# Kernel tuning notes

Hardware: AMD Instinct MI355X
Metric: run time of the kernel (lower is better)

The kernel has to match this reference:

```python
import jax, jax.numpy as jnp
import numpy as np

S, N, D = 65536, 8192, 128  # images, texts, embed dim


def setup_inputs() -> dict:
    key = jax.random.key(0)
    k1, k2, k3 = jax.random.split(key, 3)
    return {
        "image_features": jax.random.normal(k1, (S, D), dtype=jnp.float32),
        "text_features": jax.random.normal(k2, (N, D), dtype=jnp.float32),
        "key": jax.random.randint(k3, (S,), 0, N),
        "logit_scale": jnp.asarray(10.0, dtype=jnp.float32),  # already exponentiated temperature
        "logit_bias": jnp.asarray(-10.0, dtype=jnp.float32),
    }


def _l2norm(x):
    return x / (jnp.linalg.norm(x, ord=2, axis=-1, keepdims=True) + 1e-12)


def reference(image_features, text_features, key, logit_scale, logit_bias):
    s = image_features.shape[0]
    n = text_features.shape[0]
    zimg = _l2norm(image_features)           # (s, d)
    ztxt = _l2norm(text_features)            # (n, d)

    # True-positive logits: only the diagonal gather of the full (s, n) matmul is used,
    # so compute it directly as a row-wise dot product.
    tp_logits = jnp.einsum("sd,sd->s", zimg, ztxt[key]) * logit_scale + logit_bias
    pot_losses = jax.nn.softplus(-tp_logits)  # (s,)

    # Segmented argmin over images grouped by their text key (pick_best_candidate=True).
    seg_min = jax.ops.segment_min(pot_losses, key, num_segments=n)        # (n,)
    counts = jax.ops.segment_sum(jnp.ones((s,), jnp.int32), key, num_segments=n)
    valid = counts > 0                                                    # (n,)
    is_min = pot_losses == seg_min[key]
    cand_idx = jnp.where(is_min, jnp.arange(s), s)                        # first-occurrence tie-break
    best = jax.ops.segment_min(cand_idx, key, num_segments=n)             # (n,)
    best = jnp.where(valid, best, 0)

    zimg_sel = jnp.where(valid[:, None], zimg[best], 0.0)                 # (n, d)

    logits = zimg_sel @ ztxt.T * logit_scale + logit_bias                 # (n, n)
    diag = jnp.eye(n, dtype=bool)
    # labels*logits == logits on diagonal, -logits off-diagonal; softplus(-labels*logits):
    terms = jax.nn.softplus(jnp.where(diag, -logits, logits))
    mask = valid[:, None] & valid[None, :]
    num_valid = jnp.sum(valid)
    loss = jnp.sum(jnp.where(mask, terms, 0.0)) / jnp.maximum(num_valid, 1).astype(terms.dtype)
    return loss
```

## Files before the change

kernel.cpp:

```cpp
#include <hip/hip_runtime.h>
#include <stdint.h>

#define D 128

typedef __attribute__((ext_vector_type(4))) float float4v;
typedef long long frag8;

__device__ __forceinline__ float hw_exp2(float x) { return __builtin_amdgcn_exp2f(x); }
__device__ __forceinline__ float hw_log2(float x) { return __builtin_amdgcn_logf(x); }

__device__ __forceinline__ float softplus_fast(float x) {
    float e = hw_exp2(x * 1.44269504f);
    return 0.69314718f * hw_log2(1.0f + e);
}

__device__ __forceinline__ unsigned short f2fp8x2(float x, float y) {
    int p = __builtin_amdgcn_cvt_pk_fp8_f32(x, y, 0, false);
    return (unsigned short)(p & 0xFFFF);
}

__device__ __forceinline__ float dot4(float4 a, float4 b) {
    return a.x * b.x + a.y * b.y + a.z * b.z + a.w * b.w;
}

__device__ __forceinline__ void gload_lds16(const uint8_t* g, uint8_t* l) {
    __builtin_amdgcn_global_load_lds(
        (const __attribute__((address_space(1))) void*)g,
        (__attribute__((address_space(3))) void*)l, 16, 0, 0);
}

__device__ __forceinline__ int swz_col(int c, int row) {
    return c ^ ((row & 15) << 3);
}

__global__ __launch_bounds__(256) void k_prep(const float* __restrict__ img,
                                              const float* __restrict__ txt,
                                              const int* __restrict__ key,
                                              const float* __restrict__ sc,
                                              const float* __restrict__ bi,
                                              uint8_t* __restrict__ ztxt_f8,
                                              unsigned long long* __restrict__ packed,
                                              int nPack, int S) {
    const int t = threadIdx.x;
    if ((int)blockIdx.x < nPack) {
        int wave = t >> 6, lane = t & 63;
        int n = blockIdx.x * 4 + wave;
        const float2 v = *(const float2*)(txt + (size_t)n * D + lane * 2);
        float ss = v.x * v.x + v.y * v.y;
        #pragma unroll
        for (int off = 32; off; off >>= 1) ss += __shfl_xor(ss, off);
        float inv = 1.0f / (sqrtf(ss) + 1e-12f);
        *(unsigned short*)(ztxt_f8 + (size_t)n * D + swz_col(lane * 2, n)) =
            f2fp8x2(v.x * inv, v.y * inv);
    } else {
        int grp = t >> 4, gl = t & 15;
        int s = ((int)blockIdx.x - nPack) * 16 + grp;
        if (s < S) {
            int k = key[s];
            const float4* ia = (const float4*)(img + (size_t)s * D);
            const float4* tb = (const float4*)(txt + (size_t)k * D);
            float4 a0 = ia[gl], a1 = ia[16 + gl];
            float4 b0 = tb[gl], b1 = tb[16 + gl];
            float ss = dot4(a0, a0) + dot4(a1, a1);
            float dt = dot4(a0, b0) + dot4(a1, b1);
            float tt = dot4(b0, b0) + dot4(b1, b1);
            #pragma unroll
            for (int off = 8; off; off >>= 1) {
                ss += __shfl_xor(ss, off);
                dt += __shfl_xor(dt, off);
                tt += __shfl_xor(tt, off);
            }
            if (gl == 0) {
                float inv_i = 1.0f / (sqrtf(ss) + 1e-12f);
                float inv_t = 1.0f / (sqrtf(tt) + 1e-12f);
                float tp = dt * inv_i * inv_t * (*sc) + (*bi);
                float pot = softplus_fast(-tp);
                unsigned long long p =
                    ((unsigned long long)__float_as_uint(pot) << 32) | (unsigned int)s;
                atomicMin(&packed[k], p);
            }
        }
    }
}

__global__ __launch_bounds__(256) void k_select(const float* __restrict__ img,
                                               const unsigned long long* __restrict__ packed,
                                               uint8_t* __restrict__ zsel_f8,
                                               float* __restrict__ validF,
                                               double* __restrict__ partial) {
    int t = threadIdx.x;
    if (blockIdx.x == 0) partial[t] = 0.0;
    int wave = t >> 6;
    int lane = t & 63;
    int n = blockIdx.x * 4 + wave;
    unsigned long long p = packed[n];
    bool valid = (p != ~0ull);
    if (!valid) {
        if (lane == 0) validF[n] = 0.0f;
        *(unsigned short*)(zsel_f8 + (size_t)n * D + swz_col(lane * 2, n)) = 0;
        return;
    }
    int s = (int)(unsigned int)(p & 0xFFFFFFFFull);
    const float2 a = *(const float2*)(img + (size_t)s * D + lane * 2);
    float ss = a.x * a.x + a.y * a.y;
    #pragma unroll
    for (int off = 32; off; off >>= 1) ss += __shfl_xor(ss, off);
    float inv = 1.0f / (sqrtf(ss) + 1e-12f);
    *(unsigned short*)(zsel_f8 + (size_t)n * D + swz_col(lane * 2, n)) =
        f2fp8x2(a.x * inv, a.y * inv);
    if (lane == 0) validF[n] = 1.0f;
}

__global__ __launch_bounds__(256, 3) void k_gemm(const uint8_t* __restrict__ A,
                                                 const uint8_t* __restrict__ B,
                                                 const float* __restrict__ validF,
                                                 const float* __restrict__ sc,
                                                 const float* __restrict__ bi,
                                                 double* __restrict__ partial) {
    __shared__ __align__(16) uint8_t As[128 * 128];
    __shared__ __align__(16) uint8_t Bs[2][128 * 128];
    __shared__ float vI[128];
    __shared__ float vJ[512];
    __shared__ float wsum[4];

    const int t = threadIdx.x;
    const int i0 = blockIdx.y * 128;
    const int j0 = blockIdx.x * 512;

    vJ[t] = validF[j0 + t];
    vJ[t + 256] = validF[j0 + t + 256];
    if (t < 128) vI[t] = validF[i0 + t];

    const int wave = t >> 6, lane = t & 63;
    const int wm = (wave >> 1) * 64;
    const int wn = (wave & 1) * 64;
    const int lr = lane & 15;
    const int kq = (lane >> 4) * 8;
    const int swz = lr << 3;

    const uint8_t* gA = A + (size_t)i0 * D;
    const uint8_t* gB = B + (size_t)j0 * D;

    {
        #pragma unroll
        for (int j = 0; j < 4; ++j) {
            int L = wave * 4096 + j * 1024;
            gload_lds16(gA + L + lane * 16, As + L);
            gload_lds16(gB + L + lane * 16, Bs[0] + L);
        }
    }
    __syncthreads();

    const float scale = *sc, bias = *bi;
    const float sl = scale * 1.44269504f, bl = bias * 1.44269504f;
    const int rb = (lane >> 4) * 4;
    float viv[4][4];
    #pragma unroll
    for (int mi = 0; mi < 4; ++mi)
        #pragma unroll
        for (int r = 0; r < 4; ++r) viv[mi][r] = vI[wm + mi * 16 + rb + r];

    float sum = 0.0f;

    #pragma unroll
    for (int ji = 0; ji < 4; ++ji) {
        if (ji < 3) {
            const uint8_t* gS = gB + (ji + 1) * (128 * 128);
            #pragma unroll
            for (int j = 0; j < 4; ++j) {
                int L = wave * 4096 + j * 1024;
                gload_lds16(gS + L + lane * 16, Bs[(ji + 1) & 1] + L);
            }
        }
        const uint8_t* Bc = Bs[ji & 1];

        float4v acc[4][4];
        #pragma unroll
        for (int mi = 0; mi < 4; ++mi)
            #pragma unroll
            for (int ni = 0; ni < 4; ++ni)
                acc[mi][ni] = (float4v){0.f, 0.f, 0.f, 0.f};

        #pragma unroll
        for (int k0 = 0; k0 < 128; k0 += 32) {
            const int col = (k0 + kq) ^ swz;
            frag8 bf[4];
            #pragma unroll
            for (int ni = 0; ni < 4; ++ni)
                bf[ni] = *(const frag8*)(Bc + (wn + ni * 16 + lr) * 128 + col);
            #pragma unroll
            for (int mi = 0; mi < 4; ++mi) {
                frag8 af = *(const frag8*)(As + (wm + mi * 16 + lr) * 128 + col);
                #pragma unroll
                for (int ni = 0; ni < 4; ++ni)
                    acc[mi][ni] = __builtin_amdgcn_mfma_f32_16x16x32_fp8_fp8(
                        af, bf[ni], acc[mi][ni], 0, 0, 0);
            }
        }

        float vjv[4];
        #pragma unroll
        for (int ni = 0; ni < 4; ++ni) vjv[ni] = vJ[ji * 128 + wn + ni * 16 + lr];

        const int jt = blockIdx.x * 4 + ji;
        if (jt != (int)blockIdx.y) {
            #pragma unroll
            for (int ni = 0; ni < 4; ++ni) {
                float s = 0.0f;
                #pragma unroll
                for (int mi = 0; mi < 4; ++mi)
                    #pragma unroll
                    for (int r = 0; r < 4; ++r) {
                        float u = hw_exp2(fmaf(acc[mi][ni][r], sl, bl));
                        s = fmaf(u, viv[mi][r], s);
                    }
                sum = fmaf(s, vjv[ni], sum);
            }
        } else {
            #pragma unroll
            for (int ni = 0; ni < 4; ++ni) {
                float s = 0.0f;
                const int lj = wn + ni * 16 + lr;
                #pragma unroll
                for (int mi = 0; mi < 4; ++mi)
                    #pragma unroll
                    for (int r = 0; r < 4; ++r) {
                        const int li = wm + mi * 16 + rb + r;
                        float l = fmaf(acc[mi][ni][r], scale, bias);
                        float u = hw_exp2(-fabsf(l) * 1.44269504f);
                        float g = fmaxf(l, 0.0f) + fmaf(-0.5f * u, u, u);
                        if (li == lj) g -= l;
                        s = fmaf(g, viv[mi][r], s);
                    }
                sum = fmaf(s, vjv[ni], sum);
            }
        }
        if (ji < 3) __syncthreads();
    }

    #pragma unroll
    for (int off = 32; off; off >>= 1) sum += __shfl_xor(sum, off);
    if (lane == 0) wsum[wave] = sum;
    __syncthreads();
    if (t == 0) {
        float bs = wsum[0] + wsum[1] + wsum[2] + wsum[3];
        atomicAdd(&partial[(blockIdx.y * gridDim.x + blockIdx.x) & 255], (double)bs);
    }
}

__global__ __launch_bounds__(256) void k_final(const double* __restrict__ partial,
                                               const float* __restrict__ validF,
                                               float* __restrict__ out, int N) {
    __shared__ float wsum[4];
    __shared__ double dsum[4];
    int wave = threadIdx.x >> 6, lane = threadIdx.x & 63;
    float s = 0.0f;
    for (int i = threadIdx.x; i < N; i += 256) s += validF[i];
    double d = partial[threadIdx.x];
    #pragma unroll
    for (int off = 32; off; off >>= 1) {
        s += __shfl_xor(s, off);
        d += __shfl_xor(d, off);
    }
    if (lane == 0) { wsum[wave] = s; dsum[wave] = d; }
    __syncthreads();
    if (threadIdx.x == 0) {
        float nv = wsum[0] + wsum[1] + wsum[2] + wsum[3];
        if (nv < 1.0f) nv = 1.0f;
        double tot = dsum[0] + dsum[1] + dsum[2] + dsum[3];
        out[0] = (float)(tot / (double)nv);
    }
}

extern "C" void kernel_launch(void* const* d_in, const int* in_sizes, int n_in,
                              void* d_out, int out_size, void* d_ws, size_t ws_size,
                              hipStream_t stream) {
    const float* img = (const float*)d_in[0];
    const float* txt = (const float*)d_in[1];
    const int*   key = (const int*)d_in[2];
    const float* sc  = (const float*)d_in[3];
    const float* bi  = (const float*)d_in[4];
    float* out = (float*)d_out;

    const int S = in_sizes[2];
    const int N = in_sizes[1] / D;

    char* ws = (char*)d_ws;
    size_t off = 0;
    auto carve = [&](size_t bytes) {
        void* p = ws + off;
        off = (off + bytes + 255) & ~(size_t)255;
        return p;
    };
    uint8_t*            ztxt_f8 = (uint8_t*)carve((size_t)N * D);
    uint8_t*            zsel_f8 = (uint8_t*)carve((size_t)N * D);
    unsigned long long* packed  = (unsigned long long*)carve((size_t)N * sizeof(unsigned long long));
    float*              validF  = (float*)carve((size_t)N * sizeof(float));
    double*             partial = (double*)carve(256 * sizeof(double));

    hipMemsetAsync(packed, 0xFF, (size_t)N * sizeof(unsigned long long), stream);

    const int nPack = N / 4;
    k_prep<<<nPack + (S + 15) / 16, 256, 0, stream>>>(img, txt, key, sc, bi,
                                                      ztxt_f8, packed, nPack, S);
    k_select<<<N / 4, 256, 0, stream>>>(img, packed, zsel_f8, validF, partial);
    dim3 g(N / 512, N / 128);
    k_gemm<<<g, 256, 0, stream>>>(zsel_f8, ztxt_f8, validF, sc, bi, partial);
    k_final<<<1, 256, 0, stream>>>(partial, validF, out, N);
}
```

Measured before the change: 114.6 us.

## Fuse row selection into GEMM prologue and final reduction into last block

Removes the k_select and k_final kernels. Each GEMM block now gathers its 128 selected image rows, normalizes them and converts them to swizzled FP8 directly into LDS, and reads validity from the packed argmin array. The last GEMM block, found with an atomic counter, performs the final reduction. This saves two launches and the round trip of zsel/validF through global memory. In exchange, every column-block redundantly recomputes the same A rows (16x duplication), and the gather adds latency before the first MMA.

New measurement: 132.2 us. 15.4% more time.

```diff
diff --git a/kernel.cpp b/kernel.cpp
--- a/kernel.cpp
+++ b/kernel.cpp
@@ -40,9 +40,15 @@
                                               const float* __restrict__ bi,
                                               uint8_t* __restrict__ ztxt_f8,
                                               unsigned long long* __restrict__ packed,
+                                              double* __restrict__ partial,
+                                              unsigned int* __restrict__ counter,
                                               int nPack, int S) {
     const int t = threadIdx.x;
     if ((int)blockIdx.x < nPack) {
+        if (blockIdx.x == 0) {
+            partial[t] = 0.0;
+            if (t == 0) { partial[256] = 0.0; *counter = 0u; }
+        }
         int wave = t >> 6, lane = t & 63;
         int n = blockIdx.x * 4 + wave;
         const float2 v = *(const float2*)(txt + (size_t)n * D + lane * 2);
@@ -83,73 +89,80 @@
     }
 }
 
-__global__ __launch_bounds__(256) void k_select(const float* __restrict__ img,
-                                               const unsigned long long* __restrict__ packed,
-                                               uint8_t* __restrict__ zsel_f8,
-                                               float* __restrict__ validF,
-                                               double* __restrict__ partial) {
-    int t = threadIdx.x;
-    if (blockIdx.x == 0) partial[t] = 0.0;
-    int wave = t >> 6;
-    int lane = t & 63;
-    int n = blockIdx.x * 4 + wave;
-    unsigned long long p = packed[n];
-    bool valid = (p != ~0ull);
-    if (!valid) {
-        if (lane == 0) validF[n] = 0.0f;
-        *(unsigned short*)(zsel_f8 + (size_t)n * D + swz_col(lane * 2, n)) = 0;
-        return;
-    }
-    int s = (int)(unsigned int)(p & 0xFFFFFFFFull);
-    const float2 a = *(const float2*)(img + (size_t)s * D + lane * 2);
-    float ss = a.x * a.x + a.y * a.y;
-    #pragma unroll
-    for (int off = 32; off; off >>= 1) ss += __shfl_xor(ss, off);
-    float inv = 1.0f / (sqrtf(ss) + 1e-12f);
-    *(unsigned short*)(zsel_f8 + (size_t)n * D + swz_col(lane * 2, n)) =
-        f2fp8x2(a.x * inv, a.y * inv);
-    if (lane == 0) validF[n] = 1.0f;
-}
-
-__global__ __launch_bounds__(256, 3) void k_gemm(const uint8_t* __restrict__ A,
+__global__ __launch_bounds__(256, 3) void k_gemm(const float* __restrict__ img,
                                                  const uint8_t* __restrict__ B,
-                                                 const float* __restrict__ validF,
+                                                 const unsigned long long* __restrict__ packed,
                                                  const float* __restrict__ sc,
                                                  const float* __restrict__ bi,
-                                                 double* __restrict__ partial) {
+                                                 double* __restrict__ partial,
+                                                 unsigned int* __restrict__ counter,
+                                                 float* __restrict__ out, int N) {
     __shared__ __align__(16) uint8_t As[128 * 128];
     __shared__ __align__(16) uint8_t Bs[2][128 * 128];
     __shared__ float vI[128];
     __shared__ float vJ[512];
     __shared__ float wsum[4];
+    __shared__ float wcnt[4];
+    __shared__ double dred[4];
+    __shared__ int lastB;
 
     const int t = threadIdx.x;
     const int i0 = blockIdx.y * 128;
     const int j0 = blockIdx.x * 512;
 
-    vJ[t] = validF[j0 + t];
-    vJ[t + 256] = validF[j0 + t + 256];
-    if (t < 128) vI[t] = validF[i0 + t];
-
     const int wave = t >> 6, lane = t & 63;
+    const uint8_t* gB = B + (size_t)j0 * D;
+
+    {
+        #pragma unroll
+        for (int j = 0; j < 4; ++j) {
+            int L = wave * 4096 + j * 1024;
+            gload_lds16(gB + L + lane * 16, Bs[0] + L);
+        }
+    }
+
+    vJ[t]       = (packed[j0 + t] != ~0ull) ? 1.0f : 0.0f;
+    vJ[t + 256] = (packed[j0 + 256 + t] != ~0ull) ? 1.0f : 0.0f;
+
+    {
+        const int grp = t >> 4, gl = t & 15;
+        unsigned long long pk[8];
+        #pragma unroll
+        for (int it = 0; it < 8; ++it) pk[it] = packed[i0 + it * 16 + grp];
+        #pragma unroll
+        for (int it = 0; it < 8; ++it) {
+            const int row = it * 16 + grp;
+            const unsigned long long p = pk[it];
+            const bool valid = (p != ~0ull);
+            uint32_t o0 = 0, o1 = 0;
+            if (valid) {
+                int s = (int)(unsigned int)(p & 0xFFFFFFFFull);
+                const float4* ia = (const float4*)(img + (size_t)s * D);
+                float4 a0 = ia[gl], a1 = ia[16 + gl];
+                float ss = dot4(a0, a0) + dot4(a1, a1);
+                #pragma unroll
+                for (int off = 8; off; off >>= 1) ss += __shfl_xor(ss, off);
+                float inv = 1.0f / (sqrtf(ss) + 1e-12f);
+                unsigned short p01 = f2fp8x2(a0.x * inv, a0.y * inv);
+                unsigned short p23 = f2fp8x2(a0.z * inv, a0.w * inv);
+                unsigned short p45 = f2fp8x2(a1.x * inv, a1.y * inv);
+                unsigned short p67 = f2fp8x2(a1.z * inv, a1.w * inv);
+                o0 = (uint32_t)p01 | ((uint32_t)p23 << 16);
+                o1 = (uint32_t)p45 | ((uint32_t)p67 << 16);
+            }
+            if (gl == 0) vI[row] = valid ? 1.0f : 0.0f;
+            const int sw = (row & 15) << 3;
+            *(uint32_t*)(As + row * 128 + ((4 * gl) ^ sw)) = o0;
+            *(uint32_t*)(As + row * 128 + ((64 + 4 * gl) ^ sw)) = o1;
+        }
+    }
+    __syncthreads();
+
     const int wm = (wave >> 1) * 64;
     const int wn = (wave & 1) * 64;
     const int lr = lane & 15;
     const int kq = (lane >> 4) * 8;
     const int swz = lr << 3;
-
-    const uint8_t* gA = A + (size_t)i0 * D;
-    const uint8_t* gB = B + (size_t)j0 * D;
-
-    {
-        #pragma unroll
-        for (int j = 0; j < 4; ++j) {
-            int L = wave * 4096 + j * 1024;
-            gload_lds16(gA + L + lane * 16, As + L);
-            gload_lds16(gB + L + lane * 16, Bs[0] + L);
-        }
-    }
-    __syncthreads();
 
     const float scale = *sc, bias = *bi;
     const float sl = scale * 1.44269504f, bl = bias * 1.44269504f;
@@ -238,37 +251,38 @@
         if (ji < 3) __syncthreads();
     }
 
+    float vc = (blockIdx.x == 0 && t < 128) ? vI[t] : 0.0f;
     #pragma unroll
-    for (int off = 32; off; off >>= 1) sum += __shfl_xor(sum, off);
-    if (lane == 0) wsum[wave] = sum;
+    for (int off = 32; off; off >>= 1) {
+        sum += __shfl_xor(sum, off);
+        vc  += __shfl_xor(vc, off);
+    }
+    if (lane == 0) { wsum[wave] = sum; wcnt[wave] = vc; }
     __syncthreads();
     if (t == 0) {
         float bs = wsum[0] + wsum[1] + wsum[2] + wsum[3];
         atomicAdd(&partial[(blockIdx.y * gridDim.x + blockIdx.x) & 255], (double)bs);
-    }
-}
-
-__global__ __launch_bounds__(256) void k_final(const double* __restrict__ partial,
-                                               const float* __restrict__ validF,
-                                               float* __restrict__ out, int N) {
-    __shared__ float wsum[4];
-    __shared__ double dsum[4];
-    int wave = threadIdx.x >> 6, lane = threadIdx.x & 63;
-    float s = 0.0f;
-    for (int i = threadIdx.x; i < N; i += 256) s += validF[i];
-    double d = partial[threadIdx.x];
-    #pragma unroll
-    for (int off = 32; off; off >>= 1) {
-        s += __shfl_xor(s, off);
-        d += __shfl_xor(d, off);
-    }
-    if (lane == 0) { wsum[wave] = s; dsum[wave] = d; }
+        if (blockIdx.x == 0) {
+            float bc = wcnt[0] + wcnt[1] + wcnt[2] + wcnt[3];
+            atomicAdd(&partial[256], (double)bc);
+        }
+        __threadfence();
+        unsigned int v = atomicAdd(counter, 1u);
+        lastB = (v == gridDim.x * gridDim.y - 1u);
+    }
     __syncthreads();
-    if (threadIdx.x == 0) {
-        float nv = wsum[0] + wsum[1] + wsum[2] + wsum[3];
-        if (nv < 1.0f) nv = 1.0f;
-        double tot = dsum[0] + dsum[1] + dsum[2] + dsum[3];
-        out[0] = (float)(tot / (double)nv);
+    if (lastB) {
+        double ds = atomicAdd(&partial[t], 0.0);
+        #pragma unroll
+        for (int off = 32; off; off >>= 1) ds += __shfl_xor(ds, off);
+        if (lane == 0) dred[wave] = ds;
+        __syncthreads();
+        if (t == 0) {
+            double tot = dred[0] + dred[1] + dred[2] + dred[3];
+            float nv = (float)atomicAdd(&partial[256], 0.0);
+            if (nv < 1.0f) nv = 1.0f;
+            out[0] = (float)(tot / (double)nv);
+        }
     }
 }
 
@@ -293,18 +307,17 @@
         return p;
     };
     uint8_t*            ztxt_f8 = (uint8_t*)carve((size_t)N * D);
-    uint8_t*            zsel_f8 = (uint8_t*)carve((size_t)N * D);
     unsigned long long* packed  = (unsigned long long*)carve((size_t)N * sizeof(unsigned long long));
-    float*              validF  = (float*)carve((size_t)N * sizeof(float));
-    double*             partial = (double*)carve(256 * sizeof(double));
+    double*             partial = (double*)carve(257 * sizeof(double));
+    unsigned int*       counter = (unsigned int*)carve(sizeof(unsigned int));
 
     hipMemsetAsync(packed, 0xFF, (size_t)N * sizeof(unsigned long long), stream);
 
     const int nPack = N / 4;
     k_prep<<<nPack + (S + 15) / 16, 256, 0, stream>>>(img, txt, key, sc, bi,
-                                                      ztxt_f8, packed, nPack, S);
-    k_select<<<N / 4, 256, 0, stream>>>(img, packed, zsel_f8, validF, partial);
+                                                      ztxt_f8, packed, partial,
+                                                      counter, nPack, S);
     dim3 g(N / 512, N / 128);
-    k_gemm<<<g, 256, 0, stream>>>(zsel_f8, ztxt_f8, validF, sc, bi, partial);
-    k_final<<<1, 256, 0, stream>>>(partial, validF, out, N);
-}
+    k_gemm<<<g, 256, 0, stream>>>(img, ztxt_f8, packed, sc, bi,
+                                  partial, counter, out, N);
+}
```

## Make GEMM kernel persistent with atomic work queue over tiles

Applied to the files above, without the earlier changes.

Replaces the 2D grid of 1024 GEMM tiles with a persistent grid of 768 blocks that pull tile indices from a global atomic counter, which k_select resets. The tile order is column-major (by varies fastest) so consecutive blocks share the same B strip. The aim is to cut block launch overhead and tail imbalance, and to improve L2 reuse of B. In exchange it adds an atomic and a barrier per tile, and it loses the overlap of the next tile's initial loads with the previous tile's epilogue.

After: 124.5 us. +8.7%, slower.

```diff
diff --git a/kernel.cpp b/kernel.cpp
--- a/kernel.cpp
+++ b/kernel.cpp
@@ -87,9 +87,13 @@
                                                const unsigned long long* __restrict__ packed,
                                                uint8_t* __restrict__ zsel_f8,
                                                float* __restrict__ validF,
-                                               double* __restrict__ partial) {
+                                               double* __restrict__ partial,
+                                               unsigned int* __restrict__ queue) {
     int t = threadIdx.x;
-    if (blockIdx.x == 0) partial[t] = 0.0;
+    if (blockIdx.x == 0) {
+        partial[t] = 0.0;
+        if (t == 0) *queue = 0u;
+    }
     int wave = t >> 6;
     int lane = t & 63;
     int n = blockIdx.x * 4 + wave;
@@ -116,126 +120,141 @@
                                                  const float* __restrict__ validF,
                                                  const float* __restrict__ sc,
                                                  const float* __restrict__ bi,
-                                                 double* __restrict__ partial) {
+                                                 double* __restrict__ partial,
+                                                 unsigned int* __restrict__ queue,
+                                                 int N) {
     __shared__ __align__(16) uint8_t As[128 * 128];
     __shared__ __align__(16) uint8_t Bs[2][128 * 128];
     __shared__ float vI[128];
     __shared__ float vJ[512];
     __shared__ float wsum[4];
+    __shared__ int wsh;
 
     const int t = threadIdx.x;
-    const int i0 = blockIdx.y * 128;
-    const int j0 = blockIdx.x * 512;
-
-    vJ[t] = validF[j0 + t];
-    vJ[t + 256] = validF[j0 + t + 256];
-    if (t < 128) vI[t] = validF[i0 + t];
-
     const int wave = t >> 6, lane = t & 63;
     const int wm = (wave >> 1) * 64;
     const int wn = (wave & 1) * 64;
     const int lr = lane & 15;
     const int kq = (lane >> 4) * 8;
     const int swz = lr << 3;
-
-    const uint8_t* gA = A + (size_t)i0 * D;
-    const uint8_t* gB = B + (size_t)j0 * D;
-
-    {
-        #pragma unroll
-        for (int j = 0; j < 4; ++j) {
-            int L = wave * 4096 + j * 1024;
-            gload_lds16(gA + L + lane * 16, As + L);
-            gload_lds16(gB + L + lane * 16, Bs[0] + L);
-        }
-    }
-    __syncthreads();
+    const int rb = (lane >> 4) * 4;
+
+    const int nby = N >> 7;
+    const int nbx = N >> 9;
+    const int NT = nby * nbx;
 
     const float scale = *sc, bias = *bi;
     const float sl = scale * 1.44269504f, bl = bias * 1.44269504f;
-    const int rb = (lane >> 4) * 4;
-    float viv[4][4];
-    #pragma unroll
-    for (int mi = 0; mi < 4; ++mi)
-        #pragma unroll
-        for (int r = 0; r < 4; ++r) viv[mi][r] = vI[wm + mi * 16 + rb + r];
 
     float sum = 0.0f;
 
-    #pragma unroll
-    for (int ji = 0; ji < 4; ++ji) {
-        if (ji < 3) {
-            const uint8_t* gS = gB + (ji + 1) * (128 * 128);
+    for (;;) {
+        if (t == 0) wsh = (int)atomicAdd(queue, 1u);
+        __syncthreads();
+        const int w = wsh;
+        if (w >= NT) break;
+        const int by = w % nby;
+        const int bx = w / nby;
+        const int i0 = by * 128;
+        const int j0 = bx * 512;
+
+        const uint8_t* gA = A + (size_t)i0 * D;
+        const uint8_t* gB = B + (size_t)j0 * D;
+
+        {
             #pragma unroll
             for (int j = 0; j < 4; ++j) {
                 int L = wave * 4096 + j * 1024;
-                gload_lds16(gS + L + lane * 16, Bs[(ji + 1) & 1] + L);
+                gload_lds16(gA + L + lane * 16, As + L);
+                gload_lds16(gB + L + lane * 16, Bs[0] + L);
             }
         }
-        const uint8_t* Bc = Bs[ji & 1];
-
-        float4v acc[4][4];
+        vJ[t] = validF[j0 + t];
+        vJ[t + 256] = validF[j0 + t + 256];
+        if (t < 128) vI[t] = validF[i0 + t];
+        __syncthreads();
+
+        float viv[4][4];
         #pragma unroll
         for (int mi = 0; mi < 4; ++mi)
             #pragma unroll
-            for (int ni = 0; ni < 4; ++ni)
-                acc[mi][ni] = (float4v){0.f, 0.f, 0.f, 0.f};
+            for (int r = 0; r < 4; ++r) viv[mi][r] = vI[wm + mi * 16 + rb + r];
 
         #pragma unroll
-        for (int k0 = 0; k0 < 128; k0 += 32) {
-            const int col = (k0 + kq) ^ swz;
-            frag8 bf[4];
-            #pragma unroll
-            for (int ni = 0; ni < 4; ++ni)
-                bf[ni] = *(const frag8*)(Bc + (wn + ni * 16 + lr) * 128 + col);
-            #pragma unroll
-            for (int mi = 0; mi < 4; ++mi) {
-                frag8 af = *(const frag8*)(As + (wm + mi * 16 + lr) * 128 + col);
+        for (int ji = 0; ji < 4; ++ji) {
+            if (ji < 3) {
+                const uint8_t* gS = gB + (ji + 1) * (128 * 128);
+                #pragma unroll
+                for (int j = 0; j < 4; ++j) {
+                    int L = wave * 4096 + j * 1024;
+                    gload_lds16(gS + L + lane * 16, Bs[(ji + 1) & 1] + L);
+                }
+            }
+            const uint8_t* Bc = Bs[ji & 1];
+
+            float4v acc[4][4];
+            #pragma unroll
+            for (int mi = 0; mi < 4; ++mi)
                 #pragma unroll
                 for (int ni = 0; ni < 4; ++ni)
-                    acc[mi][ni] = __builtin_amdgcn_mfma_f32_16x16x32_fp8_fp8(
-                        af, bf[ni], acc[mi][ni], 0, 0, 0);
-            }
+                    acc[mi][ni] = (float4v){0.f, 0.f, 0.f, 0.f};
+
+            #pragma unroll
+            for (int k0 = 0; k0 < 128; k0 += 32) {
+                const int col = (k0 + kq) ^ swz;
+                frag8 bf[4];
+                #pragma unroll
+                for (int ni = 0; ni < 4; ++ni)
+                    bf[ni] = *(const frag8*)(Bc + (wn + ni * 16 + lr) * 128 + col);
+                #pragma unroll
+                for (int mi = 0; mi < 4; ++mi) {
+                    frag8 af = *(const frag8*)(As + (wm + mi * 16 + lr) * 128 + col);
+                    #pragma unroll
+                    for (int ni = 0; ni < 4; ++ni)
+                        acc[mi][ni] = __builtin_amdgcn_mfma_f32_16x16x32_fp8_fp8(
+                            af, bf[ni], acc[mi][ni], 0, 0, 0);
+                }
+            }
+
+            float vjv[4];
+            #pragma unroll
+            for (int ni = 0; ni < 4; ++ni) vjv[ni] = vJ[ji * 128 + wn + ni * 16 + lr];
+
+            const int jt = bx * 4 + ji;
+            if (jt != by) {
+                #pragma unroll
+                for (int ni = 0; ni < 4; ++ni) {
+                    float s = 0.0f;
+                    #pragma unroll
+                    for (int mi = 0; mi < 4; ++mi)
+                        #pragma unroll
+                        for (int r = 0; r < 4; ++r) {
+                            float u = hw_exp2(fmaf(acc[mi][ni][r], sl, bl));
+                            s = fmaf(u, viv[mi][r], s);
+                        }
+                    sum = fmaf(s, vjv[ni], sum);
+                }
+            } else {
+                #pragma unroll
+                for (int ni = 0; ni < 4; ++ni) {
+                    float s = 0.0f;
+                    const int lj = wn + ni * 16 + lr;
+                    #pragma unroll
+                    for (int mi = 0; mi < 4; ++mi)
+                        #pragma unroll
+                        for (int r = 0; r < 4; ++r) {
+                            const int li = wm + mi * 16 + rb + r;
+                            float l = fmaf(acc[mi][ni][r], scale, bias);
+                            float u = hw_exp2(-fabsf(l) * 1.44269504f);
+                            float g = fmaxf(l, 0.0f) + fmaf(-0.5f * u, u, u);
+                            if (li == lj) g -= l;
+                            s = fmaf(g, viv[mi][r], s);
+                        }
+                    sum = fmaf(s, vjv[ni], sum);
+                }
+            }
+            if (ji < 3) __syncthreads();
         }
-
-        float vjv[4];
-        #pragma unroll
-        for (int ni = 0; ni < 4; ++ni) vjv[ni] = vJ[ji * 128 + wn + ni * 16 + lr];
-
-        const int jt = blockIdx.x * 4 + ji;
-        if (jt != (int)blockIdx.y) {
-            #pragma unroll
-            for (int ni = 0; ni < 4; ++ni) {
-                float s = 0.0f;
-                #pragma unroll
-                for (int mi = 0; mi < 4; ++mi)
-                    #pragma unroll
-                    for (int r = 0; r < 4; ++r) {
-                        float u = hw_exp2(fmaf(acc[mi][ni][r], sl, bl));
-                        s = fmaf(u, viv[mi][r], s);
-                    }
-                sum = fmaf(s, vjv[ni], sum);
-            }
-        } else {
-            #pragma unroll
-            for (int ni = 0; ni < 4; ++ni) {
-                float s = 0.0f;
-                const int lj = wn + ni * 16 + lr;
-                #pragma unroll
-                for (int mi = 0; mi < 4; ++mi)
-                    #pragma unroll
-                    for (int r = 0; r < 4; ++r) {
-                        const int li = wm + mi * 16 + rb + r;
-                        float l = fmaf(acc[mi][ni][r], scale, bias);
-                        float u = hw_exp2(-fabsf(l) * 1.44269504f);
-                        float g = fmaxf(l, 0.0f) + fmaf(-0.5f * u, u, u);
-                        if (li == lj) g -= l;
-                        s = fmaf(g, viv[mi][r], s);
-                    }
-                sum = fmaf(s, vjv[ni], sum);
-            }
-        }
-        if (ji < 3) __syncthreads();
     }
 
     #pragma unroll
@@ -244,7 +263,7 @@
     __syncthreads();
     if (t == 0) {
         float bs = wsum[0] + wsum[1] + wsum[2] + wsum[3];
-        atomicAdd(&partial[(blockIdx.y * gridDim.x + blockIdx.x) & 255], (double)bs);
+        atomicAdd(&partial[blockIdx.x & 255], (double)bs);
     }
 }
 
@@ -297,14 +316,15 @@
     unsigned long long* packed  = (unsigned long long*)carve((size_t)N * sizeof(unsigned long long));
     float*              validF  = (float*)carve((size_t)N * sizeof(float));
     double*             partial = (double*)carve(256 * sizeof(double));
+    unsigned int*       queue   = (unsigned int*)carve(sizeof(unsigned int));
 
     hipMemsetAsync(packed, 0xFF, (size_t)N * sizeof(unsigned long long), stream);
 
     const int nPack = N / 4;
     k_prep<<<nPack + (S + 15) / 16, 256, 0, stream>>>(img, txt, key, sc, bi,
                                                       ztxt_f8, packed, nPack, S);
-    k_select<<<N / 4, 256, 0, stream>>>(img, packed, zsel_f8, validF, partial);
-    dim3 g(N / 512, N / 128);
-    k_gemm<<<g, 256, 0, stream>>>(zsel_f8, ztxt_f8, validF, sc, bi, partial);
+    k_select<<<N / 4, 256, 0, stream>>>(img, packed, zsel_f8, validF, partial, queue);
+    k_gemm<<<768, 256, 0, stream>>>(zsel_f8, ztxt_f8, validF, sc, bi,
+                                    partial, queue, N);
     k_final<<<1, 256, 0, stream>>>(partial, validF, out, N);
 }
```
